# Performance work log

Hardware: AMD Instinct MI355X
Metric: run time of the kernel (lower is better)

Reference implementation:

```python
import jax, jax.numpy as jnp
import numpy as np

B, SEQ, S, DIM_IN, DIM_K, DIM_V = 4, 2048, 128, 512, 64, 64
L = SEQ + 2 * S
NEG = -1e30  # stand-in for log(0) in the tril mask (finite for stable vjp)


def _layernorm(x, g, b, eps=1e-5):
    m = jnp.mean(x, axis=-1, keepdims=True)
    v = jnp.var(x, axis=-1, keepdims=True)
    return (x - m) / jnp.sqrt(v + eps) * g + b


def setup_inputs() -> dict:
    key = jax.random.key(0)
    ks = jax.random.split(key, 18)
    w = lambda k, shape, s=0.02: (jax.random.normal(k, shape, jnp.float32) * s)
    inp = {
        "x": jax.random.normal(ks[0], (B, L, DIM_IN), jnp.float32),
        "Wq": w(ks[1], (DIM_IN, DIM_K)),
        "Wk": w(ks[2], (DIM_IN, DIM_K)),
        "Wv": w(ks[3], (DIM_IN, DIM_V)),
        "Wq_s": w(ks[4], (DIM_IN, DIM_K)),
        "Wk_s": w(ks[5], (DIM_IN, DIM_K)),
        "Wv_s": w(ks[6], (DIM_IN, DIM_V)),
        "Wq_e": w(ks[7], (DIM_IN, DIM_K)),
        "Wk_e": w(ks[8], (DIM_IN, DIM_K)),
        "Wv_e": w(ks[9], (DIM_IN, DIM_V)),
        "ln_g": jnp.ones((DIM_IN,), jnp.float32),
        "ln_b": jnp.zeros((DIM_IN,), jnp.float32),
        "ln_s_g": jnp.ones((DIM_IN,), jnp.float32),
        "ln_s_b": jnp.zeros((DIM_IN,), jnp.float32),
        "ln_e_g": jnp.ones((DIM_IN,), jnp.float32),
        "ln_e_b": jnp.zeros((DIM_IN,), jnp.float32),
        "cope_emb": jax.random.normal(ks[10], (DIM_K, S), jnp.float32),
        "offset": 0,
    }
    return inp


def reference(x, Wq, Wk, Wv, Wq_s, Wk_s, Wv_s, Wq_e, Wk_e, Wv_e,
              ln_g, ln_b, ln_s_g, ln_s_b, ln_e_g, ln_e_b, cope_emb, offset):
    # extract_state: first/last state_len tokens
    xs, xm, xe = x[:, :S], x[:, S:L - S], x[:, -S:]
    xm = _layernorm(xm, ln_g, ln_b)
    xs = _layernorm(xs, ln_s_g, ln_s_b)
    xe = _layernorm(xe, ln_e_g, ln_e_b)

    q, k, v = xm @ Wq, xm @ Wk, xm @ Wv          # (B, SEQ, dk/dv)
    q_s, k_s, v_s = xs @ Wq_s, xs @ Wk_s, xs @ Wv_s
    q_e, k_e, v_e = xe @ Wq_e, xe @ Wk_e, xe @ Wv_e

    # CoPE bias over the non-state block
    logits = jnp.einsum('bqd,bkd->bqk', q, k)    # (B, SEQ, SEQ)
    gates = jax.nn.sigmoid(logits)
    pos = jnp.flip(jnp.cumsum(jnp.flip(gates, -1), axis=-1), -1)
    pos = jnp.minimum(pos, jnp.float32(S - 1))
    pos_ceil = jnp.ceil(pos).astype(jnp.int32)
    pos_floor = jnp.floor(pos).astype(jnp.int32)
    logits_int = jnp.einsum('bqd,dk->bqk', q, cope_emb)  # (B, SEQ, S)
    logits_c = jnp.take_along_axis(logits_int, pos_ceil, axis=-1)
    logits_f = jnp.take_along_axis(logits_int, pos_floor, axis=-1)
    wfrac = pos - pos_floor.astype(pos.dtype)
    bias = logits_c * wfrac + logits_f * (1.0 - wfrac)   # (B, SEQ, SEQ)

    q_full = jnp.concatenate([q_s, q, q_e], axis=1)      # (B, L, dk)
    k_full = jnp.concatenate([k_s, k, k_e], axis=1)
    v_full = jnp.concatenate([v_s, v, v_e], axis=1)

    # explicit tril log-mask bias with CoPE injected in the middle block
    tri = jnp.tril(jnp.ones((L, L), dtype=bool))
    attn_bias = jnp.where(tri, 0.0, NEG).astype(jnp.float32)
    attn_bias = jnp.broadcast_to(attn_bias, (B, L, L))
    attn_bias = attn_bias.at[:, S:L - S, S:L - S].add(bias)

    scale = 1.0 / jnp.sqrt(jnp.float32(DIM_K))
    scores = jnp.einsum('bqd,bkd->bqk', q_full, k_full) * scale + attn_bias
    att = jax.nn.softmax(scores, axis=-1)
    return jnp.einsum('bqk,bkd->bqd', att, v_full)       # (B, L, dv)
```

## Files before the change

kernel.cpp:

```cpp
#include <hip/hip_runtime.h>
#include <math.h>

#define B_    4
#define SEQ_  2048
#define S_    128
#define L_    2304
#define DIN   512
#define DK    64
#define NEGINF (-1e30f)
#define SCALE 0.125f
#define NCOLS 2176
#define NMID  8192
#define NEDGE 1024
#define LE    2304
#define PROWS 4352
#define PEPITCH 4608

typedef _Float16 f16;
typedef __attribute__((ext_vector_type(8))) _Float16 half8;
typedef __attribute__((ext_vector_type(4))) float f32x4;

union U4 { uint4 u; f16 h[8]; };

__global__ __launch_bounds__(256) void k_proj(
    const float* __restrict__ x,
    const float* __restrict__ Wq,  const float* __restrict__ Wk,  const float* __restrict__ Wv,
    const float* __restrict__ Wqs, const float* __restrict__ Wks, const float* __restrict__ Wvs,
    const float* __restrict__ Wqe, const float* __restrict__ Wke, const float* __restrict__ Wve,
    const float* __restrict__ g0, const float* __restrict__ b0,
    const float* __restrict__ gs, const float* __restrict__ bs,
    const float* __restrict__ ge, const float* __restrict__ be,
    f16* __restrict__ qsp, f16* __restrict__ ksp, f16* __restrict__ vhT)
{
    __shared__ f16 As[64 * 136];
    __shared__ f16 Bs[64 * 136];
    __shared__ float mean_s[64], rstd_s[64];
    const int tid  = threadIdx.x;
    const int row0 = blockIdx.x * 64;
    const int rseq = row0 % L_;
    const int seg  = (rseq < S_) ? 0 : (rseq >= L_ - S_) ? 2 : 1;
    const int m    = blockIdx.y;
    const float* W;
    if (m == 0)      W = (seg == 0) ? Wqs : (seg == 2) ? Wqe : Wq;
    else if (m == 1) W = (seg == 0) ? Wks : (seg == 2) ? Wke : Wk;
    else             W = (seg == 0) ? Wvs : (seg == 2) ? Wve : Wv;
    const float* gg = (seg == 0) ? gs : (seg == 2) ? ge : g0;
    const float* bb = (seg == 0) ? bs : (seg == 2) ? be : b0;

    {
        const int rr = tid >> 2, qq = tid & 3;
        const float4* xr = (const float4*)(x + (size_t)(row0 + rr) * DIN) + qq * 32;
        float s = 0.f, s2 = 0.f;
        #pragma unroll
        for (int i = 0; i < 32; ++i) {
            float4 v = xr[i];
            s  += v.x + v.y + v.z + v.w;
            s2 += v.x * v.x + v.y * v.y + v.z * v.z + v.w * v.w;
        }
        s  += __shfl_xor(s, 1);  s  += __shfl_xor(s, 2);
        s2 += __shfl_xor(s2, 1); s2 += __shfl_xor(s2, 2);
        if (qq == 0) {
            float mean = s * (1.f / DIN);
            mean_s[rr] = mean;
            rstd_s[rr] = rsqrtf(s2 * (1.f / DIN) - mean * mean + 1e-5f);
        }
    }

    const int w = tid >> 6, lane = tid & 63;
    const int cl = lane & 15, quad = lane >> 4;
    const int r0 = 32 * (w >> 1), c0 = 32 * (w & 1);

    f32x4 acc[2][2];
    #pragma unroll
    for (int i = 0; i < 2; ++i)
        #pragma unroll
        for (int j = 0; j < 2; ++j) acc[i][j] = 0.f;

    for (int kc = 0; kc < DIN; kc += 64) {
        __syncthreads();
        #pragma unroll
        for (int i = 0; i < 2; ++i) {
            int g = tid + 256 * i;
            int r = g >> 3, c8 = g & 7;
            const float* xp = x + (size_t)(row0 + r) * DIN + kc + c8 * 8;
            float4 a0 = *(const float4*)xp;
            float4 a1 = *(const float4*)(xp + 4);
            float4 gA = *(const float4*)(gg + kc + c8 * 8);
            float4 gB = *(const float4*)(gg + kc + c8 * 8 + 4);
            float4 bA = *(const float4*)(bb + kc + c8 * 8);
            float4 bB = *(const float4*)(bb + kc + c8 * 8 + 4);
            float mean = mean_s[r], rstd = rstd_s[r];
            float n[8];
            n[0] = (a0.x - mean) * rstd * gA.x + bA.x;
            n[1] = (a0.y - mean) * rstd * gA.y + bA.y;
            n[2] = (a0.z - mean) * rstd * gA.z + bA.z;
            n[3] = (a0.w - mean) * rstd * gA.w + bA.w;
            n[4] = (a1.x - mean) * rstd * gB.x + bB.x;
            n[5] = (a1.y - mean) * rstd * gB.y + bB.y;
            n[6] = (a1.z - mean) * rstd * gB.z + bB.z;
            n[7] = (a1.w - mean) * rstd * gB.w + bB.w;
            U4 hi, lo;
            #pragma unroll
            for (int j = 0; j < 8; ++j) {
                hi.h[j] = (f16)n[j];
                lo.h[j] = (f16)(n[j] - (float)hi.h[j]);
            }
            *(uint4*)(As + r * 136 + c8 * 8)      = hi.u;
            *(uint4*)(As + r * 136 + 64 + c8 * 8) = lo.u;
        }
        #pragma unroll
        for (int i = 0; i < 4; ++i) {
            int g = tid + 256 * i;
            int k = g >> 4, c4 = g & 15;
            float4 wv = ((const float4*)W)[(size_t)(kc + k) * 16 + c4];
            f16 h0 = (f16)wv.x, h1 = (f16)wv.y, h2 = (f16)wv.z, h3 = (f16)wv.w;
            Bs[(c4 * 4 + 0) * 136 + k] = h0;
            Bs[(c4 * 4 + 1) * 136 + k] = h1;
            Bs[(c4 * 4 + 2) * 136 + k] = h2;
            Bs[(c4 * 4 + 3) * 136 + k] = h3;
            Bs[(c4 * 4 + 0) * 136 + 64 + k] = (f16)(wv.x - (float)h0);
            Bs[(c4 * 4 + 1) * 136 + 64 + k] = (f16)(wv.y - (float)h1);
            Bs[(c4 * 4 + 2) * 136 + 64 + k] = (f16)(wv.z - (float)h2);
            Bs[(c4 * 4 + 3) * 136 + 64 + k] = (f16)(wv.w - (float)h3);
        }
        __syncthreads();
        #pragma unroll
        for (int h = 0; h < 2; ++h) {
            half8 ah[2], al[2], bh[2], bl[2];
            #pragma unroll
            for (int rs = 0; rs < 2; ++rs) {
                const f16* base = As + (r0 + 16 * rs + cl) * 136 + h * 32 + quad * 8;
                ah[rs] = *(const half8*)(base);
                al[rs] = *(const half8*)(base + 64);
            }
            #pragma unroll
            for (int cs = 0; cs < 2; ++cs) {
                const f16* base = Bs + (c0 + 16 * cs + cl) * 136 + h * 32 + quad * 8;
                bh[cs] = *(const half8*)(base);
                bl[cs] = *(const half8*)(base + 64);
            }
            #pragma unroll
            for (int rs = 0; rs < 2; ++rs)
                #pragma unroll
                for (int cs = 0; cs < 2; ++cs) {
                    acc[rs][cs] = __builtin_amdgcn_mfma_f32_16x16x32_f16(ah[rs], bh[cs], acc[rs][cs], 0, 0, 0);
                    if (m < 2) {
                        acc[rs][cs] = __builtin_amdgcn_mfma_f32_16x16x32_f16(ah[rs], bl[cs], acc[rs][cs], 0, 0, 0);
                        acc[rs][cs] = __builtin_amdgcn_mfma_f32_16x16x32_f16(al[rs], bh[cs], acc[rs][cs], 0, 0, 0);
                    }
                }
        }
    }

    const int bI = row0 / L_;
    const int rb = row0 - bI * L_;
    f16* sp = (m == 0) ? qsp : ksp;
    #pragma unroll
    for (int rs = 0; rs < 2; ++rs)
        #pragma unroll
        for (int cs = 0; cs < 2; ++cs)
            #pragma unroll
            for (int r = 0; r < 4; ++r) {
                int lrow = r0 + 16 * rs + quad * 4 + r;
                int col  = c0 + 16 * cs + cl;
                float v  = acc[rs][cs][r];
                size_t grow = (size_t)(row0 + lrow);
                if (m < 2) {
                    f16 hv = (f16)v;
                    sp[grow * 128 + col]      = hv;
                    sp[grow * 128 + 64 + col] = (f16)(v - (float)hv);
                } else {
                    vhT[(size_t)(bI * 64 + col) * L_ + rb + lrow] = (f16)v;
                }
            }
}

__global__ __launch_bounds__(256) void k_dots(
    const f16* __restrict__ qsp, const f16* __restrict__ ksp,
    float* __restrict__ D, float* __restrict__ G, float* __restrict__ De)
{
    const int bx = blockIdx.x, by = blockIdx.y;
    const bool edge = (bx >= 64);
    int b, q0 = 0;
    size_t qrow0;
    if (!edge) {
        if (by >= 34) return;
        b = bx >> 4;
        q0 = (bx * 128) & 2047;
        qrow0 = (size_t)b * L_ + S_ + q0;
    } else {
        int ex = bx - 64;
        b = ex >> 1;
        int half = ex & 1;
        if (half == 0 && by > 1) return;
        qrow0 = (size_t)b * L_ + (half ? 2176 : 0);
    }
    const int col0 = by * 64;
    const size_t krow0 = (size_t)b * L_ + col0;

    __shared__ f16 Qs[128 * 136];
    __shared__ f16 Ks[64 * 136];
    const int tid = threadIdx.x;

    #pragma unroll
    for (int i = 0; i < 8; ++i) {
        int g = tid + 256 * i;
        int r = g >> 4, c = g & 15;
        *(uint4*)(Qs + r * 136 + c * 8) = *(const uint4*)(qsp + (qrow0 + r) * 128 + c * 8);
    }
    #pragma unroll
    for (int i = 0; i < 4; ++i) {
        int g = tid + 256 * i;
        int r = g >> 4, c = g & 15;
        *(uint4*)(Ks + r * 136 + c * 8) = *(const uint4*)(ksp + (krow0 + r) * 128 + c * 8);
    }
    __syncthreads();

    const int w = tid >> 6, lane = tid & 63;
    const int cl = lane & 15, quad = lane >> 4;

    f32x4 acc[2][4];
    #pragma unroll
    for (int i = 0; i < 2; ++i)
        #pragma unroll
        for (int j = 0; j < 4; ++j) acc[i][j] = 0.f;

    #pragma unroll
    for (int h = 0; h < 2; ++h) {
        half8 ah[2], al[2], bh[4], bl[4];
        #pragma unroll
        for (int rs = 0; rs < 2; ++rs) {
            const f16* base = Qs + (32 * w + 16 * rs + cl) * 136 + h * 32 + quad * 8;
            ah[rs] = *(const half8*)(base);
            al[rs] = *(const half8*)(base + 64);
        }
        #pragma unroll
        for (int c = 0; c < 4; ++c) {
            const f16* base = Ks + (16 * c + cl) * 136 + h * 32 + quad * 8;
            bh[c] = *(const half8*)(base);
            bl[c] = *(const half8*)(base + 64);
        }
        #pragma unroll
        for (int rs = 0; rs < 2; ++rs)
            #pragma unroll
            for (int c = 0; c < 4; ++c) {
                acc[rs][c] = __builtin_amdgcn_mfma_f32_16x16x32_f16(ah[rs], bh[c], acc[rs][c], 0, 0, 0);
                acc[rs][c] = __builtin_amdgcn_mfma_f32_16x16x32_f16(ah[rs], bl[c], acc[rs][c], 0, 0, 0);
                acc[rs][c] = __builtin_amdgcn_mfma_f32_16x16x32_f16(al[rs], bh[c], acc[rs][c], 0, 0, 0);
            }
    }

    if (!edge) {
        const int gr0 = bx * 128;
        const bool writeD = (by < 2) || ((by - 2) <= (q0 >> 6) + 1);
        if (writeD) {
            #pragma unroll
            for (int rs = 0; rs < 2; ++rs)
                #pragma unroll
                for (int c = 0; c < 4; ++c)
                    #pragma unroll
                    for (int r = 0; r < 4; ++r) {
                        int mrow = gr0 + 32 * w + 16 * rs + quad * 4 + r;
                        int n    = col0 + 16 * c + cl;
                        D[(size_t)mrow * NCOLS + n] = acc[rs][c][r];
                    }
        }
        if (by >= 2) {
            const int chm = by - 2;
            #pragma unroll
            for (int rs = 0; rs < 2; ++rs)
                #pragma unroll
                for (int r = 0; r < 4; ++r) {
                    float s = 0.f;
                    #pragma unroll
                    for (int c = 0; c < 4; ++c)
                        s += 1.f / (1.f + __expf(-acc[rs][c][r]));
                    #pragma unroll
                    for (int off = 1; off < 16; off <<= 1) s += __shfl_xor(s, off);
                    if (cl == 0)
                        G[(size_t)(gr0 + 32 * w + 16 * rs + quad * 4 + r) * 32 + chm] = s;
                }
        }
    } else {
        const int er0 = (bx - 64) * 128;
        #pragma unroll
        for (int rs = 0; rs < 2; ++rs)
            #pragma unroll
            for (int c = 0; c < 4; ++c)
                #pragma unroll
                for (int r = 0; r < 4; ++r) {
                    int erow = er0 + 32 * w + 16 * rs + quad * 4 + r;
                    int n    = col0 + 16 * c + cl;
                    De[(size_t)erow * LE + n] = acc[rs][c][r];
                }
    }
}

__global__ __launch_bounds__(256) void k_scan(
    const f16* __restrict__ qsp, const float* __restrict__ cope,
    const float* __restrict__ G, float* __restrict__ D, float* __restrict__ De)
{
    __shared__ f16   qvh[128];
    __shared__ float li[128];
    __shared__ float Gs[32];
    __shared__ float wtot[4], wmax[4], wsum[4];
    const int tid = threadIdx.x;
    const int gr  = blockIdx.x;
    const int lane = tid & 63, wid = tid >> 6;

    if (gr < NMID) {
        const int b = gr >> 11;
        const int q = gr & 2047;
        const size_t grow = (size_t)b * L_ + S_ + q;
        const int qlim = (q & ~63) + 64;

        if (tid < 16) ((uint4*)qvh)[tid] = ((const uint4*)(qsp + grow * 128))[tid];
        if (tid >= 16 && tid < 24)
            ((float4*)Gs)[tid - 16] = ((const float4*)G)[(size_t)gr * 8 + tid - 16];
        __syncthreads();
        if (tid < 128) {
            float a = 0.f;
            #pragma unroll
            for (int d = 0; d < DK; ++d)
                a += ((float)qvh[d] + (float)qvh[64 + d]) * cope[d * S_ + tid];
            li[tid] = a;
        }

        const float* Dr = D + (size_t)gr * NCOLS;
        const int j0 = tid * 8;
        float dot[8], gte[8];
        float csum = 0.f;
        if (j0 < qlim) {
            *(float4*)&dot[0] = *(const float4*)(Dr + 128 + j0);
            *(float4*)&dot[4] = *(const float4*)(Dr + 128 + j0 + 4);
            #pragma unroll
            for (int jj = 0; jj < 8; ++jj) {
                gte[jj] = 1.f / (1.f + __expf(-dot[jj]));
                csum += gte[jj];
            }
        } else {
            #pragma unroll
            for (int jj = 0; jj < 8; ++jj) { dot[jj] = 0.f; gte[jj] = 0.f; }
        }
        float sv = (tid < 128) ? Dr[tid] * SCALE : NEGINF;

        float inc = csum;
        #pragma unroll
        for (int off = 1; off < 64; off <<= 1) {
            float u = __shfl_down(inc, off, 64);
            if (lane + off < 64) inc += u;
        }
        if (lane == 0) wtot[wid] = inc;
        __syncthreads();
        float wsuf = 0.f;
        #pragma unroll
        for (int w = 0; w < 4; ++w) if (w > wid) wsuf += wtot[w];
        float tail = 0.f;
        for (int c = (q >> 6) + 1; c < 32; ++c) tail += Gs[c];
        float run = inc - csum + wsuf + tail;

        float p8[8];
        #pragma unroll
        for (int jj = 7; jj >= 0; --jj) {
            run += gte[jj];
            float pos = fminf(run, (float)(S_ - 1));
            float pfl = floorf(pos);
            int ic  = (int)ceilf(pos);
            int ifl = (int)pfl;
            float w = pos - pfl;
            float bias = li[ic] * w + li[ifl] * (1.f - w);
            p8[jj] = (j0 + jj <= q) ? dot[jj] * SCALE + bias : NEGINF;
        }

        float mx = sv;
        #pragma unroll
        for (int jj = 0; jj < 8; ++jj) mx = fmaxf(mx, p8[jj]);
        #pragma unroll
        for (int off = 1; off < 64; off <<= 1) mx = fmaxf(mx, __shfl_xor(mx, off));
        if (lane == 0) wmax[wid] = mx;
        __syncthreads();
        mx = fmaxf(fmaxf(wmax[0], wmax[1]), fmaxf(wmax[2], wmax[3]));

        float lsum = 0.f;
        float e8[8];
        #pragma unroll
        for (int jj = 0; jj < 8; ++jj) {
            e8[jj] = __expf(p8[jj] - mx);
            lsum += e8[jj];
        }
        float es = 0.f;
        if (tid < 128) { es = __expf(sv - mx); lsum += es; }
        #pragma unroll
        for (int off = 1; off < 64; off <<= 1) lsum += __shfl_xor(lsum, off);
        if (lane == 0) wsum[wid] = lsum;
        __syncthreads();
        float inv = 1.f / (wsum[0] + wsum[1] + wsum[2] + wsum[3]);

        f16* pb = (f16*)D + (size_t)gr * PROWS;
        if (j0 < qlim) {
            U4 o;
            #pragma unroll
            for (int jj = 0; jj < 8; ++jj) o.h[jj] = (f16)(e8[jj] * inv);
            *(uint4*)(pb + 128 + j0) = o.u;
        }
        if (tid < 128) pb[tid] = (f16)(es * inv);
    } else {
        const int er = gr - NMID;
        const int r  = er & 255;
        const int Q  = (r < 128) ? r : (2048 + r);
        const size_t rowoff = (size_t)er * LE;

        float v[9];
        #pragma unroll
        for (int i = 0; i < 9; ++i) {
            int j = tid + 256 * i;
            float d = De[rowoff + j];
            v[i] = (j <= Q) ? d * SCALE : NEGINF;
        }
        float mx = v[0];
        #pragma unroll
        for (int i = 1; i < 9; ++i) mx = fmaxf(mx, v[i]);
        #pragma unroll
        for (int off = 1; off < 64; off <<= 1) mx = fmaxf(mx, __shfl_xor(mx, off));
        if (lane == 0) wmax[wid] = mx;
        __syncthreads();
        mx = fmaxf(fmaxf(wmax[0], wmax[1]), fmaxf(wmax[2], wmax[3]));

        float lsum = 0.f;
        #pragma unroll
        for (int i = 0; i < 9; ++i) {
            v[i] = __expf(v[i] - mx);
            lsum += v[i];
        }
        #pragma unroll
        for (int off = 1; off < 64; off <<= 1) lsum += __shfl_xor(lsum, off);
        if (lane == 0) wsum[wid] = lsum;
        __syncthreads();
        float inv = 1.f / (wsum[0] + wsum[1] + wsum[2] + wsum[3]);

        f16* pe = (f16*)De + (size_t)er * PEPITCH;
        #pragma unroll
        for (int i = 0; i < 9; ++i)
            pe[tid + 256 * i] = (f16)(v[i] * inv);
    }
}

__global__ __launch_bounds__(256) void k_pv(
    const f16* __restrict__ Pmid, const f16* __restrict__ Pedge,
    const f16* __restrict__ vhT,
    float* __restrict__ Opart, float* __restrict__ Oe)
{
    __shared__ f16 Ps[64 * 72];
    __shared__ f16 Vt[64 * 72];
    const int tid = threadIdx.x;
    const int bx  = blockIdx.x;
    const int ks  = blockIdx.y;
    const bool edge = (bx >= 128);

    const f16* Pb;
    size_t pitch;
    int row0, b, cap, cmax;
    float* outp;
    if (!edge) {
        row0 = bx * 64;
        b = row0 >> 11;
        int q0 = row0 & 2047;
        Pb = Pmid; pitch = PROWS; cap = 34;
        cmax = (191 + q0) >> 6;
        outp = Opart + (size_t)ks * NMID * DK;
    } else {
        row0 = (bx - 128) * 64;
        b = row0 >> 8;
        int r0 = row0 & 255;
        Pb = Pedge; pitch = PEPITCH; cap = 36;
        int Qmax = (r0 < 128) ? (r0 + 63) : (2048 + r0 + 63);
        cmax = Qmax >> 6;
        outp = Oe + (size_t)ks * NEDGE * DK;
    }
    const int c_beg = ks * 9;
    int c_end = c_beg + 9;
    if (c_end > cap) c_end = cap;
    if (c_end > cmax + 1) c_end = cmax + 1;

    const int w = tid >> 6, lane = tid & 63;
    const int cl = lane & 15, quad = lane >> 4;
    f32x4 acc[4];
    #pragma unroll
    for (int c = 0; c < 4; ++c) acc[c] = 0.f;

    for (int ch = c_beg; ch < c_end; ++ch) {
        __syncthreads();
        #pragma unroll
        for (int i = 0; i < 2; ++i) {
            int g = tid + 256 * i;
            int r = g >> 3, c = g & 7;
            *(uint4*)(Ps + r * 72 + c * 8) =
                *(const uint4*)(Pb + (size_t)(row0 + r) * pitch + ch * 64 + c * 8);
            *(uint4*)(Vt + r * 72 + c * 8) =
                *(const uint4*)(vhT + (size_t)(b * 64 + r) * L_ + ch * 64 + c * 8);
        }
        __syncthreads();
        #pragma unroll
        for (int h = 0; h < 2; ++h) {
            half8 a = *(const half8*)(Ps + (16 * w + cl) * 72 + h * 32 + quad * 8);
            #pragma unroll
            for (int c = 0; c < 4; ++c) {
                half8 bv = *(const half8*)(Vt + (16 * c + cl) * 72 + h * 32 + quad * 8);
                acc[c] = __builtin_amdgcn_mfma_f32_16x16x32_f16(a, bv, acc[c], 0, 0, 0);
            }
        }
    }
    #pragma unroll
    for (int c = 0; c < 4; ++c)
        #pragma unroll
        for (int r = 0; r < 4; ++r) {
            int mrow = row0 + 16 * w + quad * 4 + r;
            int n    = 16 * c + cl;
            outp[(size_t)mrow * DK + n] = acc[c][r];
        }
}

__global__ __launch_bounds__(256) void k_merge(
    const float* __restrict__ Opart, const float* __restrict__ Oe,
    float* __restrict__ out)
{
    const int e = blockIdx.x * 256 + threadIdx.x;
    if (e < NMID * DK) {
        const int gr = e >> 6, c = e & 63;
        const int b  = gr >> 11, q = gr & 2047;
        const int NP = NMID * DK;
        float s = Opart[e] + Opart[e + NP] + Opart[e + 2 * NP] + Opart[e + 3 * NP];
        out[((size_t)b * L_ + S_ + q) * DK + c] = s;
    } else {
        const int e2 = e - NMID * DK;
        const int er = e2 >> 6, c = e2 & 63;
        const int b  = er >> 8, r = er & 255;
        const int gQ = (r < 128) ? r : (2048 + r);
        const int NP = NEDGE * DK;
        float s = Oe[e2] + Oe[e2 + NP] + Oe[e2 + 2 * NP] + Oe[e2 + 3 * NP];
        out[((size_t)b * L_ + gQ) * DK + c] = s;
    }
}

extern "C" void kernel_launch(void* const* d_in, const int* in_sizes, int n_in,
                              void* d_out, int out_size, void* d_ws, size_t ws_size,
                              hipStream_t stream)
{
    const float* x    = (const float*)d_in[0];
    const float* Wq   = (const float*)d_in[1];
    const float* Wk   = (const float*)d_in[2];
    const float* Wv   = (const float*)d_in[3];
    const float* Wqs  = (const float*)d_in[4];
    const float* Wks  = (const float*)d_in[5];
    const float* Wvs  = (const float*)d_in[6];
    const float* Wqe  = (const float*)d_in[7];
    const float* Wke  = (const float*)d_in[8];
    const float* Wve  = (const float*)d_in[9];
    const float* g0   = (const float*)d_in[10];
    const float* b0   = (const float*)d_in[11];
    const float* gs   = (const float*)d_in[12];
    const float* bs   = (const float*)d_in[13];
    const float* ge   = (const float*)d_in[14];
    const float* be   = (const float*)d_in[15];
    const float* cope = (const float*)d_in[16];

    const size_t NR = (size_t)B_ * L_;
    f16*   qsp   = (f16*)d_ws;
    f16*   ksp   = qsp + NR * 128;
    f16*   vhT   = ksp + NR * 128;
    float* G     = (float*)(vhT + NR * 64);
    float* Opart = G + (size_t)NMID * 32;
    float* Oe    = Opart + (size_t)4 * NMID * DK;
    float* D     = Oe + (size_t)4 * NEDGE * DK;
    float* De    = D + (size_t)NMID * NCOLS;
    float* out   = (float*)d_out;

    k_proj<<<dim3(144, 3), 256, 0, stream>>>(x, Wq, Wk, Wv, Wqs, Wks, Wvs,
                                             Wqe, Wke, Wve, g0, b0, gs, bs,
                                             ge, be, qsp, ksp, vhT);
    k_dots<<<dim3(72, 36), 256, 0, stream>>>(qsp, ksp, D, G, De);
    k_scan<<<NMID + NEDGE, 256, 0, stream>>>(qsp, cope, G, D, De);
    k_pv  <<<dim3(144, 4), 256, 0, stream>>>((const f16*)D, (const f16*)De,
                                             vhT, Opart, Oe);
    k_merge<<<(NMID + NEDGE) * DK / 256, 256, 0, stream>>>(Opart, Oe, out);
}
```

Baseline: 201.7 us.

## Store QK dot matrices in fp16 and fuse split-K merge via atomics

The raw QK dot products D and De are now written as fp16 instead of fp32, halving the traffic of the largest intermediate between k_dots and k_scan. The per-chunk gate suffix sums are precomputed once in shared memory, so the block-wide scan becomes an 8-lane segmented scan. The separate k_merge pass and its partial-output buffers are removed: k_pv atomically adds its split-K partials into a zeroed output, and blocks with an empty chunk range exit early. Rounding the logits to fp16 before the sigmoid gates and softmax costs accuracy, and fp32 atomics make the summation order nondeterministic.

```diff
diff --git a/kernel.cpp b/kernel.cpp
--- a/kernel.cpp
+++ b/kernel.cpp
@@ -13,8 +13,6 @@
 #define NMID  8192
 #define NEDGE 1024
 #define LE    2304
-#define PROWS 4352
-#define PEPITCH 4608
 
 typedef _Float16 f16;
 typedef __attribute__((ext_vector_type(8))) _Float16 half8;
@@ -177,7 +175,7 @@
 
 __global__ __launch_bounds__(256) void k_dots(
     const f16* __restrict__ qsp, const f16* __restrict__ ksp,
-    float* __restrict__ D, float* __restrict__ G, float* __restrict__ De)
+    f16* __restrict__ D, float* __restrict__ G, f16* __restrict__ De)
 {
     const int bx = blockIdx.x, by = blockIdx.y;
     const bool edge = (bx >= 64);
@@ -262,7 +260,7 @@
                     for (int r = 0; r < 4; ++r) {
                         int mrow = gr0 + 32 * w + 16 * rs + quad * 4 + r;
                         int n    = col0 + 16 * c + cl;
-                        D[(size_t)mrow * NCOLS + n] = acc[rs][c][r];
+                        D[(size_t)mrow * NCOLS + n] = (f16)acc[rs][c][r];
                     }
         }
         if (by >= 2) {
@@ -291,19 +289,20 @@
                 for (int r = 0; r < 4; ++r) {
                     int erow = er0 + 32 * w + 16 * rs + quad * 4 + r;
                     int n    = col0 + 16 * c + cl;
-                    De[(size_t)erow * LE + n] = acc[rs][c][r];
+                    De[(size_t)erow * LE + n] = (f16)acc[rs][c][r];
                 }
     }
 }
 
 __global__ __launch_bounds__(256) void k_scan(
     const f16* __restrict__ qsp, const float* __restrict__ cope,
-    const float* __restrict__ G, float* __restrict__ D, float* __restrict__ De)
+    const float* __restrict__ G, f16* __restrict__ D, f16* __restrict__ De)
 {
     __shared__ f16   qvh[128];
     __shared__ float li[128];
     __shared__ float Gs[32];
-    __shared__ float wtot[4], wmax[4], wsum[4];
+    __shared__ float Gsf[32];
+    __shared__ float wmax[4], wsum[4];
     const int tid = threadIdx.x;
     const int gr  = blockIdx.x;
     const int lane = tid & 63, wid = tid >> 6;
@@ -325,16 +324,23 @@
                 a += ((float)qvh[d] + (float)qvh[64 + d]) * cope[d * S_ + tid];
             li[tid] = a;
         }
-
-        const float* Dr = D + (size_t)gr * NCOLS;
+        if (tid >= 128 && tid < 160) {
+            int c = tid - 128;
+            float s = 0.f;
+            for (int cc = c + 1; cc < 32; ++cc) s += Gs[cc];
+            Gsf[c] = s;
+        }
+
+        f16* Dr = D + (size_t)gr * NCOLS;
         const int j0 = tid * 8;
+        const int cg = tid >> 3, sl = tid & 7;
         float dot[8], gte[8];
         float csum = 0.f;
         if (j0 < qlim) {
-            *(float4*)&dot[0] = *(const float4*)(Dr + 128 + j0);
-            *(float4*)&dot[4] = *(const float4*)(Dr + 128 + j0 + 4);
+            U4 t; t.u = *(const uint4*)(Dr + 128 + j0);
             #pragma unroll
             for (int jj = 0; jj < 8; ++jj) {
+                dot[jj] = (float)t.h[jj];
                 gte[jj] = 1.f / (1.f + __expf(-dot[jj]));
                 csum += gte[jj];
             }
@@ -342,22 +348,16 @@
             #pragma unroll
             for (int jj = 0; jj < 8; ++jj) { dot[jj] = 0.f; gte[jj] = 0.f; }
         }
-        float sv = (tid < 128) ? Dr[tid] * SCALE : NEGINF;
+        float sv = (tid < 128) ? (float)Dr[tid] * SCALE : NEGINF;
 
         float inc = csum;
         #pragma unroll
-        for (int off = 1; off < 64; off <<= 1) {
-            float u = __shfl_down(inc, off, 64);
-            if (lane + off < 64) inc += u;
-        }
-        if (lane == 0) wtot[wid] = inc;
-        __syncthreads();
-        float wsuf = 0.f;
-        #pragma unroll
-        for (int w = 0; w < 4; ++w) if (w > wid) wsuf += wtot[w];
-        float tail = 0.f;
-        for (int c = (q >> 6) + 1; c < 32; ++c) tail += Gs[c];
-        float run = inc - csum + wsuf + tail;
+        for (int off = 1; off < 8; off <<= 1) {
+            float u = __shfl_down(inc, off, 8);
+            if (sl + off < 8) inc += u;
+        }
+        __syncthreads();
+        float run = (inc - csum) + Gsf[cg];
 
         float p8[8];
         #pragma unroll
@@ -396,25 +396,24 @@
         __syncthreads();
         float inv = 1.f / (wsum[0] + wsum[1] + wsum[2] + wsum[3]);
 
-        f16* pb = (f16*)D + (size_t)gr * PROWS;
         if (j0 < qlim) {
             U4 o;
             #pragma unroll
             for (int jj = 0; jj < 8; ++jj) o.h[jj] = (f16)(e8[jj] * inv);
-            *(uint4*)(pb + 128 + j0) = o.u;
-        }
-        if (tid < 128) pb[tid] = (f16)(es * inv);
+            *(uint4*)(Dr + 128 + j0) = o.u;
+        }
+        if (tid < 128) Dr[tid] = (f16)(es * inv);
     } else {
         const int er = gr - NMID;
         const int r  = er & 255;
         const int Q  = (r < 128) ? r : (2048 + r);
-        const size_t rowoff = (size_t)er * LE;
+        f16* Er = De + (size_t)er * LE;
 
         float v[9];
         #pragma unroll
         for (int i = 0; i < 9; ++i) {
             int j = tid + 256 * i;
-            float d = De[rowoff + j];
+            float d = (float)Er[j];
             v[i] = (j <= Q) ? d * SCALE : NEGINF;
         }
         float mx = v[0];
@@ -438,17 +437,15 @@
         __syncthreads();
         float inv = 1.f / (wsum[0] + wsum[1] + wsum[2] + wsum[3]);
 
-        f16* pe = (f16*)De + (size_t)er * PEPITCH;
         #pragma unroll
         for (int i = 0; i < 9; ++i)
-            pe[tid + 256 * i] = (f16)(v[i] * inv);
+            Er[tid + 256 * i] = (f16)(v[i] * inv);
     }
 }
 
 __global__ __launch_bounds__(256) void k_pv(
     const f16* __restrict__ Pmid, const f16* __restrict__ Pedge,
-    const f16* __restrict__ vhT,
-    float* __restrict__ Opart, float* __restrict__ Oe)
+    const f16* __restrict__ vhT, float* __restrict__ out)
 {
     __shared__ f16 Ps[64 * 72];
     __shared__ f16 Vt[64 * 72];
@@ -460,27 +457,25 @@
     const f16* Pb;
     size_t pitch;
     int row0, b, cap, cmax;
-    float* outp;
     if (!edge) {
         row0 = bx * 64;
         b = row0 >> 11;
         int q0 = row0 & 2047;
-        Pb = Pmid; pitch = PROWS; cap = 34;
+        Pb = Pmid; pitch = NCOLS; cap = 34;
         cmax = (191 + q0) >> 6;
-        outp = Opart + (size_t)ks * NMID * DK;
     } else {
         row0 = (bx - 128) * 64;
         b = row0 >> 8;
         int r0 = row0 & 255;
-        Pb = Pedge; pitch = PEPITCH; cap = 36;
+        Pb = Pedge; pitch = LE; cap = 36;
         int Qmax = (r0 < 128) ? (r0 + 63) : (2048 + r0 + 63);
         cmax = Qmax >> 6;
-        outp = Oe + (size_t)ks * NEDGE * DK;
     }
     const int c_beg = ks * 9;
     int c_end = c_beg + 9;
     if (c_end > cap) c_end = cap;
     if (c_end > cmax + 1) c_end = cmax + 1;
+    if (c_end <= c_beg) return;
 
     const int w = tid >> 6, lane = tid & 63;
     const int cl = lane & 15, quad = lane >> 4;
@@ -514,32 +509,18 @@
     for (int c = 0; c < 4; ++c)
         #pragma unroll
         for (int r = 0; r < 4; ++r) {
-            int mrow = row0 + 16 * w + quad * 4 + r;
+            int lrow = row0 + 16 * w + quad * 4 + r;
             int n    = 16 * c + cl;
-            outp[(size_t)mrow * DK + n] = acc[c][r];
-        }
-}
-
-__global__ __launch_bounds__(256) void k_merge(
-    const float* __restrict__ Opart, const float* __restrict__ Oe,
-    float* __restrict__ out)
-{
-    const int e = blockIdx.x * 256 + threadIdx.x;
-    if (e < NMID * DK) {
-        const int gr = e >> 6, c = e & 63;
-        const int b  = gr >> 11, q = gr & 2047;
-        const int NP = NMID * DK;
-        float s = Opart[e] + Opart[e + NP] + Opart[e + 2 * NP] + Opart[e + 3 * NP];
-        out[((size_t)b * L_ + S_ + q) * DK + c] = s;
-    } else {
-        const int e2 = e - NMID * DK;
-        const int er = e2 >> 6, c = e2 & 63;
-        const int b  = er >> 8, r = er & 255;
-        const int gQ = (r < 128) ? r : (2048 + r);
-        const int NP = NEDGE * DK;
-        float s = Oe[e2] + Oe[e2 + NP] + Oe[e2 + 2 * NP] + Oe[e2 + 3 * NP];
-        out[((size_t)b * L_ + gQ) * DK + c] = s;
-    }
+            size_t orow;
+            if (!edge) {
+                orow = (size_t)b * L_ + S_ + (lrow & 2047);
+            } else {
+                int rr = lrow & 255;
+                int gQ = (rr < 128) ? rr : (2048 + rr);
+                orow = (size_t)b * L_ + gQ;
+            }
+            atomicAdd(&out[orow * DK + n], acc[c][r]);
+        }
 }
 
 extern "C" void kernel_launch(void* const* d_in, const int* in_sizes, int n_in,
@@ -565,22 +546,19 @@
     const float* cope = (const float*)d_in[16];
 
     const size_t NR = (size_t)B_ * L_;
-    f16*   qsp   = (f16*)d_ws;
-    f16*   ksp   = qsp + NR * 128;
-    f16*   vhT   = ksp + NR * 128;
-    float* G     = (float*)(vhT + NR * 64);
-    float* Opart = G + (size_t)NMID * 32;
-    float* Oe    = Opart + (size_t)4 * NMID * DK;
-    float* D     = Oe + (size_t)4 * NEDGE * DK;
-    float* De    = D + (size_t)NMID * NCOLS;
-    float* out   = (float*)d_out;
-
+    f16*   qsp = (f16*)d_ws;
+    f16*   ksp = qsp + NR * 128;
+    f16*   vhT = ksp + NR * 128;
+    float* G   = (float*)(vhT + NR * 64);
+    f16*   D   = (f16*)(G + (size_t)NMID * 32);
+    f16*   De  = D + (size_t)NMID * NCOLS;
+    float* out = (float*)d_out;
+
+    hipMemsetAsync(out, 0, (size_t)out_size * sizeof(float), stream);
     k_proj<<<dim3(144, 3), 256, 0, stream>>>(x, Wq, Wk, Wv, Wqs, Wks, Wvs,
                                              Wqe, Wke, Wve, g0, b0, gs, bs,
                                              ge, be, qsp, ksp, vhT);
     k_dots<<<dim3(72, 36), 256, 0, stream>>>(qsp, ksp, D, G, De);
     k_scan<<<NMID + NEDGE, 256, 0, stream>>>(qsp, cope, G, D, De);
-    k_pv  <<<dim3(144, 4), 256, 0, stream>>>((const f16*)D, (const f16*)De,
-                                             vhT, Opart, Oe);
-    k_merge<<<(NMID + NEDGE) * DK / 256, 256, 0, stream>>>(Opart, Oe, out);
+    k_pv  <<<dim3(144, 4), 256, 0, stream>>>(D, De, vhT, out);
 }
```

Measured after the change: 199.2 us. No clear change (-1.2%).
